# Kernel optimization log

Hardware: AMD Instinct MI355X
Metric: run time of the kernel (lower is better)

## Reference

```python
import jax, jax.numpy as jnp
import numpy as np

DIM = 256


def setup_inputs() -> dict:
    key = jax.random.key(0)
    ks = jax.random.split(key, 10)
    d = DIM
    inp = {
        "agent": jax.random.normal(ks[0], (64, d), dtype=jnp.float32),
        "x": jax.random.normal(ks[1], (8, 4096, d), dtype=jnp.float32),
        # parameters (stored as [in, out]; y = x @ W + b)
        "W_qkv": jax.random.normal(ks[2], (d, 3 * d), dtype=jnp.float32) * (d ** -0.5),
        "b_qkv": jnp.zeros((3 * d,), dtype=jnp.float32),
        "W_agent": jax.random.normal(ks[3], (d, 2 * d), dtype=jnp.float32) * (d ** -0.5),
        "b_agent": jnp.zeros((2 * d,), dtype=jnp.float32),
        "W_fc1": jax.random.normal(ks[4], (d, d), dtype=jnp.float32) * (d ** -0.5),
        "b_fc1": jnp.zeros((d,), dtype=jnp.float32),
        "W_fc2": jax.random.normal(ks[5], (d, d), dtype=jnp.float32) * (d ** -0.5),
        "b_fc2": jnp.zeros((d,), dtype=jnp.float32),
    }
    return inp


def reference(agent, x, W_qkv, b_qkv, W_agent, b_agent, W_fc1, b_fc1, W_fc2, b_fc2):
    d = x.shape[-1]
    scale = d ** -0.5
    # qkv projection of tokens: [B,N,3d] -> q,k,v each [B,N,d]
    qkv = x @ W_qkv + b_qkv
    q, k, v = jnp.split(qkv, 3, axis=-1)
    # agent projection: [K,2d] -> q_agent,k_agent each [K,d]
    ag = agent @ W_agent + b_agent
    q_agent, k_agent = jnp.split(ag, 2, axis=-1)
    # stage 1: agents attend over tokens -> [B,K,N]
    attn1 = jax.nn.softmax(jnp.einsum('kd,bnd->bkn', q_agent, k) * scale, axis=-1)
    va = jnp.einsum('bkn,bnd->bkd', attn1, v)  # [B,K,d]
    va = va @ W_fc1 + b_fc1
    # stage 2: tokens attend over agents -> [B,N,K]
    attn2 = jax.nn.softmax(jnp.einsum('bnd,kd->bnk', q, k_agent) * scale, axis=-1)
    out = jnp.einsum('bnk,bkd->bnd', attn2, va)  # [B,N,d]
    out = out @ W_fc2 + b_fc2
    return out + x
```

## Files before the change

### kernel.cpp

```cpp
#include <hip/hip_runtime.h>
#include <stdint.h>
#include <string.h>

#define BB 8
#define NN 4096
#define DD 256
#define SCALE 0.0625f
#define XS 264
#define XT 72

using frag_ab = __attribute__((ext_vector_type(8))) short;
using frag_cd = __attribute__((ext_vector_type(4))) float;

__device__ __forceinline__ unsigned short f2bf(float f) {
    union { float f; unsigned u; } a; a.f = f;
    unsigned r = a.u + 0x7FFFu + ((a.u >> 16) & 1u);
    return (unsigned short)(r >> 16);
}
__device__ __forceinline__ float bf2f(unsigned short h) {
    union { unsigned u; float f; } a; a.u = ((unsigned)h) << 16;
    return a.f;
}
__device__ __forceinline__ int xsw(int tok, int d) {
    const int e = ((tok >> 3) & 3) << 1;
    return tok * XS + (d & 7) + (((d >> 3) ^ e) << 3);
}

__global__ __launch_bounds__(256) void k_setup(
    const float* __restrict__ agent, const float* __restrict__ Wag,
    const float* __restrict__ bag, const float* __restrict__ Wqkv,
    const float* __restrict__ bqkv, const float* __restrict__ Wfc1,
    const float* __restrict__ bfc1, const float* __restrict__ Wfc2,
    unsigned short* __restrict__ P12t, float* __restrict__ c2,
    unsigned short* __restrict__ W3b, float* __restrict__ b3)
{
    __shared__ float arow[256];
    __shared__ float red[4][256];
    float* redf = &red[0][0];
    const int bx = blockIdx.x, tid = threadIdx.x;
    const int w = tid >> 6, lane = tid & 63;
    const int c4 = lane * 4;
    if (bx < 128) {
        const int c = bx;
        const int woff = (c < 64) ? 256 : 0;
        const int aoff = (c < 64) ? 0 : 256;
        const int row = c & 63;
        {
            float p4[4] = {0.f, 0.f, 0.f, 0.f};
            for (int oo = 0; oo < 64; ++oo) {
                const int o = w * 64 + oo;
                const float ao = agent[row * 256 + o];
                float4 wv = *(const float4*)&Wag[o * 512 + aoff + c4];
                p4[0] += ao * wv.x; p4[1] += ao * wv.y;
                p4[2] += ao * wv.z; p4[3] += ao * wv.w;
            }
#pragma unroll
            for (int jj = 0; jj < 4; ++jj) red[w][c4 + jj] = p4[jj];
        }
        __syncthreads();
        arow[tid] = bag[aoff + tid] + red[0][tid] + red[1][tid] + red[2][tid] + red[3][tid];
        __syncthreads();
        {
            const float4* wr = (const float4*)&Wqkv[(size_t)tid * 768 + woff];
            float s = 0.f;
#pragma unroll 4
            for (int o4 = 0; o4 < 64; ++o4) {
                float4 v = wr[o4];
                s += v.x * arow[o4 * 4] + v.y * arow[o4 * 4 + 1] +
                     v.z * arow[o4 * 4 + 2] + v.w * arow[o4 * 4 + 3];
            }
            P12t[(size_t)c * 256 + tid] = f2bf(SCALE * s);
        }
        if (c >= 64) {
            __syncthreads();
            redf[tid] = bqkv[woff + tid] * arow[tid];
            __syncthreads();
            for (int st = 128; st; st >>= 1) {
                if (tid < st) redf[tid] += redf[tid + st];
                __syncthreads();
            }
            if (tid == 0) c2[c - 64] = SCALE * redf[0];
        }
    } else {
        const int i = bx - 128;
        const bool isb3 = (bx == 384);
        {
            float p4[4] = {0.f, 0.f, 0.f, 0.f};
            for (int oo = 0; oo < 64; ++oo) {
                const int o = w * 64 + oo;
                const float wv = isb3 ? bqkv[512 + o] : Wqkv[(size_t)i * 768 + 512 + o];
                float4 f1 = *(const float4*)&Wfc1[o * 256 + c4];
                p4[0] += wv * f1.x; p4[1] += wv * f1.y;
                p4[2] += wv * f1.z; p4[3] += wv * f1.w;
            }
#pragma unroll
            for (int jj = 0; jj < 4; ++jj) red[w][c4 + jj] = p4[jj];
        }
        __syncthreads();
        arow[tid] = (isb3 ? bfc1[tid] : 0.f) +
                    red[0][tid] + red[1][tid] + red[2][tid] + red[3][tid];
        __syncthreads();
        {
            float p4[4] = {0.f, 0.f, 0.f, 0.f};
            for (int kk = 0; kk < 64; ++kk) {
                const int k = w * 64 + kk;
                const float av = arow[k];
                float4 f2 = *(const float4*)&Wfc2[k * 256 + c4];
                p4[0] += av * f2.x; p4[1] += av * f2.y;
                p4[2] += av * f2.z; p4[3] += av * f2.w;
            }
#pragma unroll
            for (int jj = 0; jj < 4; ++jj) red[w][c4 + jj] = p4[jj];
        }
        __syncthreads();
        const float o4 = red[0][tid] + red[1][tid] + red[2][tid] + red[3][tid];
        if (isb3) b3[tid] = o4;
        else      W3b[(size_t)i * 256 + tid] = f2bf(o4);
    }
}

__global__ __launch_bounds__(512) void k_fuse(
    const float* __restrict__ x, const unsigned short* __restrict__ P12t,
    const float* __restrict__ c2, unsigned short* __restrict__ p2b,
    unsigned short* __restrict__ part, float* __restrict__ statS)
{
    __shared__ unsigned short xtile[64 * XS];
    __shared__ unsigned short Pl[64 * XT];
    __shared__ float Ss[4][64];
    const int s = blockIdx.x, b = blockIdx.y;
    const int n0 = s * 64;
    const int tid = threadIdx.x;
    const int w = tid >> 6, lane = tid & 63;
    const int ml = lane & 15, q = lane >> 4;
    const int rt = w & 3, cg = w >> 2;

#pragma unroll
    for (int p = 0; p < 8; ++p) {
        int idx = p * 512 + tid;
        int tok = idx >> 6, d = (idx & 63) * 4;
        float4 v = *(const float4*)&x[(size_t)(b * 4096 + n0 + tok) * 256 + d];
        unsigned short u[4] = {f2bf(v.x), f2bf(v.y), f2bf(v.z), f2bf(v.w)};
        uint2 pk; memcpy(&pk, u, 8);
        *(uint2*)&xtile[xsw(tok, d)] = pk;
    }
    __syncthreads();

    frag_ab afr[8];
#pragma unroll
    for (int kb4 = 0; kb4 < 4; ++kb4)
#pragma unroll
        for (int ks = 0; ks < 2; ++ks)
            afr[kb4 * 2 + ks] =
                *(const frag_ab*)&xtile[xsw(rt * 16 + ml, kb4 * 64 + ks * 32 + q * 8)];

    frag_cd acc1[4];
#pragma unroll
    for (int j = 0; j < 4; ++j)
#pragma unroll
        for (int r = 0; r < 4; ++r) acc1[j][r] = 0.f;

    for (int kb4 = 0; kb4 < 4; ++kb4) {
#pragma unroll
        for (int ks = 0; ks < 2; ++ks) {
            const int kk = kb4 * 64 + ks * 32 + q * 8;
            const frag_ab a = afr[kb4 * 2 + ks];
#pragma unroll
            for (int j = 0; j < 4; ++j) {
                frag_ab bf = *(const frag_ab*)
                    &P12t[(size_t)(cg * 64 + j * 16 + ml) * 256 + kk];
                acc1[j] = __builtin_amdgcn_mfma_f32_16x16x32_bf16(a, bf, acc1[j], 0, 0, 0);
            }
        }
    }

    if (cg == 1) {
        float cc[4];
#pragma unroll
        for (int j = 0; j < 4; ++j) cc[j] = c2[j * 16 + ml];
#pragma unroll
        for (int r = 0; r < 4; ++r) {
            float e[4], sum = 0.f;
#pragma unroll
            for (int j = 0; j < 4; ++j) {
                e[j] = __expf(acc1[j][r] + cc[j]);
                sum += e[j];
            }
#pragma unroll
            for (int mask = 1; mask <= 8; mask <<= 1) sum += __shfl_xor(sum, mask);
            float inv = 1.f / sum;
            const int tok = n0 + rt * 16 + q * 4 + r;
#pragma unroll
            for (int j = 0; j < 4; ++j)
                p2b[(size_t)(b * 4096 + tok) * 64 + j * 16 + ml] = f2bf(e[j] * inv);
        }
    } else {
        float e1[4][4];
#pragma unroll
        for (int j = 0; j < 4; ++j) {
#pragma unroll
            for (int r = 0; r < 4; ++r) e1[j][r] = __expf(acc1[j][r]);
            float sj = e1[j][0] + e1[j][1] + e1[j][2] + e1[j][3];
            sj += __shfl_xor(sj, 16);
            sj += __shfl_xor(sj, 32);
            if (lane < 16) Ss[rt][j * 16 + ml] = sj;
        }
#pragma unroll
        for (int j = 0; j < 4; ++j)
#pragma unroll
            for (int r = 0; r < 4; ++r)
                Pl[(j * 16 + ml) * XT + rt * 16 + q * 4 + r] = f2bf(e1[j][r]);
    }
    __syncthreads();

    if (tid < 64)
        statS[(size_t)(b * 64 + tid) * 64 + s] =
            Ss[0][tid] + Ss[1][tid] + Ss[2][tid] + Ss[3][tid];

    {
        const int af = w & 3, dh = w >> 2;
        frag_cd acc2[8];
#pragma unroll
        for (int i = 0; i < 8; ++i)
#pragma unroll
            for (int r = 0; r < 4; ++r) acc2[i][r] = 0.f;
#pragma unroll
        for (int ks = 0; ks < 2; ++ks) {
            const int kk = ks * 32 + q * 8;
            frag_ab a = *(const frag_ab*)&Pl[(af * 16 + ml) * XT + kk];
#pragma unroll
            for (int i = 0; i < 8; ++i) {
                const int d = dh * 128 + i * 16 + ml;
                unsigned short u[8];
#pragma unroll
                for (int t = 0; t < 8; ++t) u[t] = xtile[xsw(kk + t, d)];
                frag_ab bf; memcpy(&bf, u, 16);
                acc2[i] = __builtin_amdgcn_mfma_f32_16x16x32_bf16(a, bf, acc2[i], 0, 0, 0);
            }
        }
#pragma unroll
        for (int i = 0; i < 8; ++i)
#pragma unroll
            for (int r = 0; r < 4; ++r)
                part[(size_t)((s * 8 + b) * 64 + af * 16 + q * 4 + r) * 256 +
                     dh * 128 + i * 16 + ml] = f2bf(acc2[i][r]);
    }
}

__global__ __launch_bounds__(256) void k_fc(
    const unsigned short* __restrict__ part, const float* __restrict__ statS,
    const unsigned short* __restrict__ W3b, const float* __restrict__ b3,
    unsigned short* __restrict__ va3t)
{
    __shared__ float red[4][256];
    __shared__ float rowb[256];
    __shared__ float rs[64];
    const int row = blockIdx.x, tid = threadIdx.x;
    const int b = row >> 6, agc = row & 63;
    const int w = tid >> 6, lane = tid & 63;
    const int c4 = lane * 4;
    {
        float p4[4] = {0.f, 0.f, 0.f, 0.f};
        for (int ss = 0; ss < 16; ++ss) {
            const int s = w * 16 + ss;
            uint2 pk = *(const uint2*)&part[(size_t)((s * 8 + b) * 64 + agc) * 256 + c4];
            unsigned short u[4]; memcpy(u, &pk, 8);
#pragma unroll
            for (int k = 0; k < 4; ++k) p4[k] += bf2f(u[k]);
        }
#pragma unroll
        for (int k = 0; k < 4; ++k) red[w][c4 + k] = p4[k];
    }
    if (tid < 64) rs[tid] = statS[(size_t)(b * 64 + agc) * 64 + tid];
    __syncthreads();
    float tot = 0.f;
#pragma unroll
    for (int t = 0; t < 64; ++t) tot += rs[t];
    rowb[tid] = (red[0][tid] + red[1][tid] + red[2][tid] + red[3][tid]) / tot;
    __syncthreads();
    {
        float p4[4] = {0.f, 0.f, 0.f, 0.f};
        for (int kk = 0; kk < 64; ++kk) {
            const int k = w * 64 + kk;
            const float rv = rowb[k];
            uint2 pk = *(const uint2*)&W3b[(size_t)k * 256 + c4];
            unsigned short u[4]; memcpy(u, &pk, 8);
#pragma unroll
            for (int jj = 0; jj < 4; ++jj) p4[jj] += rv * bf2f(u[jj]);
        }
#pragma unroll
        for (int jj = 0; jj < 4; ++jj) red[w][c4 + jj] = p4[jj];
    }
    __syncthreads();
    const float s2 = b3[tid] + red[0][tid] + red[1][tid] + red[2][tid] + red[3][tid];
    va3t[(size_t)(b * 256 + tid) * 64 + agc] = f2bf(s2);
}

__global__ __launch_bounds__(256) void k_stage2(
    const unsigned short* __restrict__ p2b, const unsigned short* __restrict__ va3t,
    const float* __restrict__ x, const float* __restrict__ bfc2,
    float* __restrict__ out)
{
    const int n0 = blockIdx.x * 32, b = blockIdx.y;
    const int tid = threadIdx.x;
    const int w = tid >> 6, lane = tid & 63;
    const int ml = lane & 15, q = lane >> 4;

    frag_cd acc[4][2];
#pragma unroll
    for (int i = 0; i < 4; ++i)
#pragma unroll
        for (int j = 0; j < 2; ++j)
#pragma unroll
            for (int r = 0; r < 4; ++r) acc[i][j][r] = 0.f;
#pragma unroll
    for (int ks = 0; ks < 2; ++ks) {
        const int kk = ks * 32 + q * 8;
        frag_ab a[4], bf[2];
#pragma unroll
        for (int i = 0; i < 4; ++i)
            a[i] = *(const frag_ab*)&va3t[(size_t)(b * 256 + w * 64 + i * 16 + ml) * 64 + kk];
#pragma unroll
        for (int j = 0; j < 2; ++j)
            bf[j] = *(const frag_ab*)&p2b[(size_t)(b * 4096 + n0 + j * 16 + ml) * 64 + kk];
#pragma unroll
        for (int i = 0; i < 4; ++i)
#pragma unroll
            for (int j = 0; j < 2; ++j)
                acc[i][j] = __builtin_amdgcn_mfma_f32_16x16x32_bf16(
                    a[i], bf[j], acc[i][j], 0, 0, 0);
    }

#pragma unroll
    for (int i = 0; i < 4; ++i) {
        const int d0 = w * 64 + i * 16 + q * 4;
        float4 bias = *(const float4*)&bfc2[d0];
#pragma unroll
        for (int j = 0; j < 2; ++j) {
            const int tok = n0 + j * 16 + ml;
            size_t ad = (size_t)(b * 4096 + tok) * 256 + d0;
            float4 xr = *(const float4*)&x[ad];
            float4 o;
            o.x = acc[i][j][0] + bias.x + xr.x;
            o.y = acc[i][j][1] + bias.y + xr.y;
            o.z = acc[i][j][2] + bias.z + xr.z;
            o.w = acc[i][j][3] + bias.w + xr.w;
            *(float4*)&out[ad] = o;
        }
    }
}

extern "C" void kernel_launch(void* const* d_in, const int* in_sizes, int n_in,
                              void* d_out, int out_size, void* d_ws, size_t ws_size,
                              hipStream_t stream) {
    const float* agent = (const float*)d_in[0];
    const float* x     = (const float*)d_in[1];
    const float* Wqkv  = (const float*)d_in[2];
    const float* bqkv  = (const float*)d_in[3];
    const float* Wag   = (const float*)d_in[4];
    const float* bag   = (const float*)d_in[5];
    const float* Wfc1  = (const float*)d_in[6];
    const float* bfc1  = (const float*)d_in[7];
    const float* Wfc2  = (const float*)d_in[8];
    const float* bfc2  = (const float*)d_in[9];
    float* out = (float*)d_out;

    char* wsp = (char*)d_ws;
    size_t off = 0;
    unsigned short* p2b  = (unsigned short*)(wsp + off); off += (size_t)BB * NN * 64 * 2;
    unsigned short* part = (unsigned short*)(wsp + off); off += (size_t)64 * BB * 64 * 256 * 2;
    float* statS = (float*)(wsp + off); off += (size_t)BB * 64 * 64 * 4;
    unsigned short* P12t = (unsigned short*)(wsp + off); off += (size_t)128 * 256 * 2;
    float* c2   = (float*)(wsp + off); off += 256 * 4;
    unsigned short* W3b = (unsigned short*)(wsp + off); off += (size_t)256 * 256 * 2;
    float* b3   = (float*)(wsp + off); off += 256 * 4;
    unsigned short* va3t = (unsigned short*)(wsp + off); off += (size_t)BB * DD * 64 * 2;

    k_setup<<<385, 256, 0, stream>>>(agent, Wag, bag, Wqkv, bqkv, Wfc1, bfc1, Wfc2,
                                     P12t, c2, W3b, b3);
    k_fuse<<<dim3(64, BB), 512, 0, stream>>>(x, P12t, c2, p2b, part, statS);
    k_fc<<<512, 256, 0, stream>>>(part, statS, W3b, b3, va3t);
    k_stage2<<<dim3(128, BB), 256, 0, stream>>>(p2b, va3t, x, bfc2, out);
}
```

Before: 173.6 us.

## Halve k_fuse token tile to 32 to double block count across CUs

Shrinks the k_fuse token tile from 64 to 32 tokens per block with 256 threads, launching 128x8 blocks instead of 64x8. The stage-1 partial AV product is restructured so each wave covers a 64-column slice and all four agent fragments over a single K=32 step. The point is better CU occupancy and load balance on a 256-CU part. The cost is that the partial-sum buffer and statS double, so k_fc must reduce 128 partials per row, which adds global traffic.

Result: slower. 183.1 us (+5.5%).

```diff
diff --git a/kernel.cpp b/kernel.cpp
--- a/kernel.cpp
+++ b/kernel.cpp
@@ -7,7 +7,7 @@
 #define DD 256
 #define SCALE 0.0625f
 #define XS 264
-#define XT 72
+#define PLS 40
 
 using frag_ab = __attribute__((ext_vector_type(8))) short;
 using frag_cd = __attribute__((ext_vector_type(4))) float;
@@ -119,24 +119,24 @@
     }
 }
 
-__global__ __launch_bounds__(512) void k_fuse(
+__global__ __launch_bounds__(256) void k_fuse(
     const float* __restrict__ x, const unsigned short* __restrict__ P12t,
     const float* __restrict__ c2, unsigned short* __restrict__ p2b,
     unsigned short* __restrict__ part, float* __restrict__ statS)
 {
-    __shared__ unsigned short xtile[64 * XS];
-    __shared__ unsigned short Pl[64 * XT];
-    __shared__ float Ss[4][64];
+    __shared__ unsigned short xtile[32 * XS];
+    __shared__ unsigned short Pl[64 * PLS];
+    __shared__ float Ss[2][64];
     const int s = blockIdx.x, b = blockIdx.y;
-    const int n0 = s * 64;
+    const int n0 = s * 32;
     const int tid = threadIdx.x;
     const int w = tid >> 6, lane = tid & 63;
     const int ml = lane & 15, q = lane >> 4;
-    const int rt = w & 3, cg = w >> 2;
+    const int rt = w & 1, cg = w >> 1;
 
 #pragma unroll
     for (int p = 0; p < 8; ++p) {
-        int idx = p * 512 + tid;
+        int idx = p * 256 + tid;
         int tok = idx >> 6, d = (idx & 63) * 4;
         float4 v = *(const float4*)&x[(size_t)(b * 4096 + n0 + tok) * 256 + d];
         unsigned short u[4] = {f2bf(v.x), f2bf(v.y), f2bf(v.z), f2bf(v.w)};
@@ -208,41 +208,36 @@
         for (int j = 0; j < 4; ++j)
 #pragma unroll
             for (int r = 0; r < 4; ++r)
-                Pl[(j * 16 + ml) * XT + rt * 16 + q * 4 + r] = f2bf(e1[j][r]);
+                Pl[(j * 16 + ml) * PLS + rt * 16 + q * 4 + r] = f2bf(e1[j][r]);
     }
     __syncthreads();
 
     if (tid < 64)
-        statS[(size_t)(b * 64 + tid) * 64 + s] =
-            Ss[0][tid] + Ss[1][tid] + Ss[2][tid] + Ss[3][tid];
+        statS[(size_t)(b * 64 + tid) * 128 + s] = Ss[0][tid] + Ss[1][tid];
 
     {
-        const int af = w & 3, dh = w >> 2;
-        frag_cd acc2[8];
-#pragma unroll
-        for (int i = 0; i < 8; ++i)
-#pragma unroll
-            for (int r = 0; r < 4; ++r) acc2[i][r] = 0.f;
-#pragma unroll
-        for (int ks = 0; ks < 2; ++ks) {
-            const int kk = ks * 32 + q * 8;
-            frag_ab a = *(const frag_ab*)&Pl[(af * 16 + ml) * XT + kk];
-#pragma unroll
-            for (int i = 0; i < 8; ++i) {
-                const int d = dh * 128 + i * 16 + ml;
-                unsigned short u[8];
-#pragma unroll
-                for (int t = 0; t < 8; ++t) u[t] = xtile[xsw(kk + t, d)];
-                frag_ab bf; memcpy(&bf, u, 16);
-                acc2[i] = __builtin_amdgcn_mfma_f32_16x16x32_bf16(a, bf, acc2[i], 0, 0, 0);
-            }
-        }
-#pragma unroll
-        for (int i = 0; i < 8; ++i)
-#pragma unroll
-            for (int r = 0; r < 4; ++r)
-                part[(size_t)((s * 8 + b) * 64 + af * 16 + q * 4 + r) * 256 +
-                     dh * 128 + i * 16 + ml] = f2bf(acc2[i][r]);
+        const int kk = q * 8;
+        frag_ab a[4];
+#pragma unroll
+        for (int af = 0; af < 4; ++af)
+            a[af] = *(const frag_ab*)&Pl[(af * 16 + ml) * PLS + kk];
+#pragma unroll
+        for (int i = 0; i < 4; ++i) {
+            const int d = w * 64 + i * 16 + ml;
+            unsigned short u[8];
+#pragma unroll
+            for (int t = 0; t < 8; ++t) u[t] = xtile[xsw(kk + t, d)];
+            frag_ab bf; memcpy(&bf, u, 16);
+#pragma unroll
+            for (int af = 0; af < 4; ++af) {
+                frag_cd acc2 = {0.f, 0.f, 0.f, 0.f};
+                acc2 = __builtin_amdgcn_mfma_f32_16x16x32_bf16(a[af], bf, acc2, 0, 0, 0);
+#pragma unroll
+                for (int r = 0; r < 4; ++r)
+                    part[(size_t)((s * 8 + b) * 64 + af * 16 + q * 4 + r) * 256 + d]
+                        = f2bf(acc2[r]);
+            }
+        }
     }
 }
 
@@ -253,15 +248,15 @@
 {
     __shared__ float red[4][256];
     __shared__ float rowb[256];
-    __shared__ float rs[64];
+    __shared__ float rs[128];
     const int row = blockIdx.x, tid = threadIdx.x;
     const int b = row >> 6, agc = row & 63;
     const int w = tid >> 6, lane = tid & 63;
     const int c4 = lane * 4;
     {
         float p4[4] = {0.f, 0.f, 0.f, 0.f};
-        for (int ss = 0; ss < 16; ++ss) {
-            const int s = w * 16 + ss;
+        for (int ss = 0; ss < 32; ++ss) {
+            const int s = w * 32 + ss;
             uint2 pk = *(const uint2*)&part[(size_t)((s * 8 + b) * 64 + agc) * 256 + c4];
             unsigned short u[4]; memcpy(u, &pk, 8);
 #pragma unroll
@@ -270,11 +265,11 @@
 #pragma unroll
         for (int k = 0; k < 4; ++k) red[w][c4 + k] = p4[k];
     }
-    if (tid < 64) rs[tid] = statS[(size_t)(b * 64 + agc) * 64 + tid];
+    if (tid < 128) rs[tid] = statS[(size_t)(b * 64 + agc) * 128 + tid];
     __syncthreads();
     float tot = 0.f;
 #pragma unroll
-    for (int t = 0; t < 64; ++t) tot += rs[t];
+    for (int t = 0; t < 128; ++t) tot += rs[t];
     rowb[tid] = (red[0][tid] + red[1][tid] + red[2][tid] + red[3][tid]) / tot;
     __syncthreads();
     {
@@ -367,8 +362,8 @@
     char* wsp = (char*)d_ws;
     size_t off = 0;
     unsigned short* p2b  = (unsigned short*)(wsp + off); off += (size_t)BB * NN * 64 * 2;
-    unsigned short* part = (unsigned short*)(wsp + off); off += (size_t)64 * BB * 64 * 256 * 2;
-    float* statS = (float*)(wsp + off); off += (size_t)BB * 64 * 64 * 4;
+    unsigned short* part = (unsigned short*)(wsp + off); off += (size_t)128 * BB * 64 * 256 * 2;
+    float* statS = (float*)(wsp + off); off += (size_t)BB * 64 * 128 * 4;
     unsigned short* P12t = (unsigned short*)(wsp + off); off += (size_t)128 * 256 * 2;
     float* c2   = (float*)(wsp + off); off += 256 * 4;
     unsigned short* W3b = (unsigned short*)(wsp + off); off += (size_t)256 * 256 * 2;
@@ -377,7 +372,7 @@
 
     k_setup<<<385, 256, 0, stream>>>(agent, Wag, bag, Wqkv, bqkv, Wfc1, bfc1, Wfc2,
                                      P12t, c2, W3b, b3);
-    k_fuse<<<dim3(64, BB), 512, 0, stream>>>(x, P12t, c2, p2b, part, statS);
+    k_fuse<<<dim3(128, BB), 256, 0, stream>>>(x, P12t, c2, p2b, part, statS);
     k_fc<<<512, 256, 0, stream>>>(part, statS, W3b, b3, va3t);
     k_stage2<<<dim3(128, BB), 256, 0, stream>>>(p2b, va3t, x, bfc2, out);
 }
```
